# Kernel optimization log

Measured on AMD Instinct MI355X. Metric: run time of the kernel, lower is better.

The kernel has to match this reference:

```python
import jax, jax.numpy as jnp
import numpy as np

N_NODES = 50000
N_EDGES = 1600000
D = 128  # input_dim == hidden_dim


def glorot(key, shape):
    lim = float(np.sqrt(6.0 / (shape[0] + shape[1])))
    return jax.random.uniform(key, shape, jnp.float32, -lim, lim)


def setup_inputs() -> dict:
    key = jax.random.key(0)
    ks = jax.random.split(key, 10)
    x = jax.random.normal(ks[0], (N_NODES, D), jnp.float32)
    edge_index = jax.random.randint(ks[1], (2, N_EDGES), 0, N_NODES, jnp.int64)
    edge_attr = jax.random.normal(ks[2], (N_EDGES, D), jnp.float32)
    # SAGEConv params per layer: lin_l (W,b), lin_r (W, no bias)
    W1l = glorot(ks[3], (D, D)); b1l = jnp.zeros((D,), jnp.float32)
    W1r = glorot(ks[4], (D, D))
    W2l = glorot(ks[5], (D, D)); b2l = jnp.zeros((D,), jnp.float32)
    W2r = glorot(ks[6], (D, D))
    return {"x": x, "edge_index": edge_index, "edge_attr": edge_attr,
            "W1l": W1l, "b1l": b1l, "W1r": W1r,
            "W2l": W2l, "b2l": b2l, "W2r": W2r}


def sage_layer(z, src, dst, edge_attr, Wl, bl, Wr):
    # message: gather x_j, add edge_attr, relu  -> [E, D]
    msg = jax.nn.relu(z[src] + edge_attr)
    # mean aggregation at destination nodes
    agg = jax.ops.segment_sum(msg, dst, num_segments=N_NODES)
    cnt = jax.ops.segment_sum(jnp.ones((dst.shape[0], 1), z.dtype), dst,
                              num_segments=N_NODES)
    agg = agg / jnp.maximum(cnt, 1.0)
    # lin_l(agg) + lin_r(x) (root weight, no bias on lin_r)
    return agg @ Wl + bl + z @ Wr


def reference(x, edge_index, edge_attr, W1l, b1l, W1r, W2l, b2l, W2r):
    src, dst = edge_index[0], edge_index[1]
    z = sage_layer(x, src, dst, edge_attr, W1l, b1l, W1r)
    z = jax.nn.relu(z)  # activation between layers; dropout=0, normalize='none'
    z = sage_layer(z, src, dst, edge_attr, W2l, b2l, W2r)
    return z
```

## Files before the change

### kernel.cpp

```cpp
#include <hip/hip_runtime.h>

#define D 128

typedef __attribute__((ext_vector_type(8))) short bf16x8;
typedef __attribute__((ext_vector_type(4))) float f32x4;
typedef __attribute__((ext_vector_type(4))) unsigned short u16x4;
typedef __attribute__((ext_vector_type(4))) unsigned char u8x4;

__device__ inline unsigned short f2bf(float f) {
    union { float f; unsigned u; } v; v.f = f;
    unsigned r = v.u + 0x7FFF + ((v.u >> 16) & 1);
    return (unsigned short)(r >> 16);
}
__device__ inline float bf2f(unsigned short h) {
    union { unsigned u; float f; } v; v.u = ((unsigned)h) << 16; return v.f;
}
__device__ inline unsigned char f2fp8(float f) {
    unsigned u = __float_as_uint(f);
    unsigned s = (u >> 31) << 7;
    unsigned r = (u & 0x7fffffffu) + 0x7FFFF + ((u >> 20) & 1);
    int e = (int)(r >> 23) - 127;
    if (e < -6) return (unsigned char)s;
    return (unsigned char)(s | ((unsigned)(e + 7) << 3) | ((r >> 20) & 7));
}
__device__ inline float fp82f(unsigned c) {
    unsigned ef = (c >> 3) & 0xF, m = c & 7, s = c >> 7;
    unsigned nb = (s << 31) | ((ef + 120) << 23) | (m << 20);
    float nv = __uint_as_float(nb);
    float sv = (s ? -0.001953125f : 0.001953125f) * (float)m;
    return ef ? nv : sv;
}


__global__ __launch_bounds__(256) void prep_kernel(const float* __restrict__ x,
                                                   unsigned short* __restrict__ xb, int n4,
                                                   const int* __restrict__ dst,
                                                   int* __restrict__ cnt, int E,
                                                   const float* __restrict__ W1l,
                                                   const float* __restrict__ W1r,
                                                   const float* __restrict__ W2l,
                                                   const float* __restrict__ W2r,
                                                   unsigned short* __restrict__ Wt1,
                                                   unsigned short* __restrict__ Wt2,
                                                   int CAST_B, int CNT_B) {
    int b = blockIdx.x, tid = threadIdx.x;
    if (b < CAST_B) {
        int i = b * 256 + tid;
        if (i < n4) {
            float4 v = reinterpret_cast<const float4*>(x)[i];
            ushort4 r;
            r.x = f2bf(v.x); r.y = f2bf(v.y); r.z = f2bf(v.z); r.w = f2bf(v.w);
            reinterpret_cast<ushort4*>(xb)[i] = r;
        }
    } else if (b < CAST_B + CNT_B) {
        int e = (b - CAST_B) * 256 + tid;
        if (e < E) atomicAdd(&cnt[dst[e]], 1);
    } else {
        int c = b - CAST_B - CNT_B;
        int k = tid;
        float v1 = (k < 128) ? W1l[k * 128 + c] : W1r[(k - 128) * 128 + c];
        float v2 = (k < 128) ? W2l[k * 128 + c] : W2r[(k - 128) * 128 + c];
        Wt1[c * 256 + k] = f2bf(v1);
        Wt2[c * 256 + k] = f2bf(v2);
    }
}


__global__ __launch_bounds__(256) void psum_kernel(const int* __restrict__ cnt,
                                                   int* __restrict__ bsum, int n) {
    __shared__ int wsh[4];
    int b = blockIdx.x, tid = threadIdx.x;
    int i0 = b * 1024 + tid * 4;
    int s = 0;
    #pragma unroll
    for (int j = 0; j < 4; ++j) { int i = i0 + j; if (i < n) s += cnt[i]; }
    #pragma unroll
    for (int d = 1; d < 64; d <<= 1) s += __shfl_xor(s, d, 64);
    if ((tid & 63) == 0) wsh[tid >> 6] = s;
    __syncthreads();
    if (tid == 0) bsum[b] = wsh[0] + wsh[1] + wsh[2] + wsh[3];
}

__global__ __launch_bounds__(64) void bscan_kernel(const int* __restrict__ bsum,
                                                   int* __restrict__ bpre, int nb) {
    int t = threadIdx.x;
    int v = (t < nb) ? bsum[t] : 0;
    int sc = v;
    #pragma unroll
    for (int d = 1; d < 64; d <<= 1) { int u = __shfl_up(sc, d, 64); if (t >= d) sc += u; }
    if (t < nb) bpre[t] = sc - v;
}

__global__ __launch_bounds__(256) void fscan_kernel(const int* __restrict__ cnt,
                                                    const int* __restrict__ bpre,
                                                    int* __restrict__ off,
                                                    int* __restrict__ cursor, int n) {
    __shared__ int wsum[4];
    int b = blockIdx.x, tid = threadIdx.x;
    int lane = tid & 63, wv = tid >> 6;
    int i0 = b * 1024 + tid * 4;
    int v[4]; int s = 0;
    #pragma unroll
    for (int j = 0; j < 4; ++j) { int i = i0 + j; v[j] = (i < n) ? cnt[i] : 0; s += v[j]; }
    int sc = s;
    #pragma unroll
    for (int d = 1; d < 64; d <<= 1) { int u = __shfl_up(sc, d, 64); if (lane >= d) sc += u; }
    if (lane == 63) wsum[wv] = sc;
    __syncthreads();
    int wp = 0;
    for (int j = 0; j < wv; ++j) wp += wsum[j];
    int base = bpre[b] + wp + sc - s;
    #pragma unroll
    for (int j = 0; j < 4; ++j) {
        int i = i0 + j;
        if (i < n) { cursor[i] = base; off[i + 1] = base + v[j]; }
        base += v[j];
    }
    if (b == 0 && tid == 0) off[0] = 0;
}

__global__ __launch_bounds__(256) void fill_kernel(const int* __restrict__ src,
                                                   const int* __restrict__ dst,
                                                   int* __restrict__ cursor,
                                                   long long* __restrict__ pairs, int E) {
    int e = blockIdx.x * 256 + threadIdx.x;
    if (e < E) {
        int d = dst[e];
        int slot = atomicAdd(&cursor[d], 1);
        long long v = (long long)(unsigned)src[e] | ((long long)e << 32);
        __builtin_nontemporal_store(v, &pairs[slot]);
    }
}


template <int EA_FP8>
__global__ __launch_bounds__(256) void aggregate_kernel(const unsigned short* __restrict__ featb,
                                                        const float* __restrict__ ea,
                                                        unsigned char* __restrict__ eaq,
                                                        const int* __restrict__ off,
                                                        const long long* __restrict__ pairs,
                                                        unsigned short* __restrict__ aggb,
                                                        int N) {
    int nd = blockIdx.x * 4 + (threadIdx.x >> 6);
    if (nd >= N) return;
    int t = threadIdx.x & 63;
    int half = t >> 5, l32 = t & 31;
    int s = off[nd], e = off[nd + 1];
    float a0 = 0.f, a1 = 0.f, a2 = 0.f, a3 = 0.f;

    for (int b = s; b < e; b += 64) {
        int cnt = min(64, e - b);
        long long prl = (b + t < e) ? __builtin_nontemporal_load(&pairs[b + t]) : 0LL;
        int psrc = (int)prl;
        int peid = (int)(prl >> 32);

        auto fetch = [&](int idx, f32x4& ev, u16x4& xv) {
            int sidx = __shfl(psrc, idx, 64);
            int q = b + idx;
            if (EA_FP8) {
                u8x4 eq = __builtin_nontemporal_load(
                    reinterpret_cast<const u8x4*>(&eaq[(size_t)q * D + l32 * 4]));
                ev[0] = fp82f(eq[0]); ev[1] = fp82f(eq[1]);
                ev[2] = fp82f(eq[2]); ev[3] = fp82f(eq[3]);
            } else {
                int eidx = __shfl(peid, idx, 64);
                ev = __builtin_nontemporal_load(
                    reinterpret_cast<const f32x4*>(&ea[(size_t)eidx * D + l32 * 4]));
                u8x4 wq;
                wq[0] = f2fp8(ev[0]); wq[1] = f2fp8(ev[1]);
                wq[2] = f2fp8(ev[2]); wq[3] = f2fp8(ev[3]);
                __builtin_nontemporal_store(wq,
                    reinterpret_cast<u8x4*>(&eaq[(size_t)q * D + l32 * 4]));
            }
            xv = *reinterpret_cast<const u16x4*>(&featb[(size_t)sidx * D + l32 * 4]);
        };
        auto accum = [&](const f32x4& ev, const u16x4& xv) {
            a0 += fmaxf(bf2f(xv[0]) + ev[0], 0.f);
            a1 += fmaxf(bf2f(xv[1]) + ev[1], 0.f);
            a2 += fmaxf(bf2f(xv[2]) + ev[2], 0.f);
            a3 += fmaxf(bf2f(xv[3]) + ev[3], 0.f);
        };

        int p = 0;
        for (; p + 8 <= cnt; p += 8) {
            f32x4 e0, e1, e2, e3; u16x4 x0, x1, x2, x3;
            fetch(p + half, e0, x0);
            fetch(p + 2 + half, e1, x1);
            fetch(p + 4 + half, e2, x2);
            fetch(p + 6 + half, e3, x3);
            accum(e0, x0); accum(e1, x1); accum(e2, x2); accum(e3, x3);
        }
        if (p + 4 <= cnt) {
            f32x4 e0, e1; u16x4 x0, x1;
            fetch(p + half, e0, x0);
            fetch(p + 2 + half, e1, x1);
            accum(e0, x0); accum(e1, x1);
            p += 4;
        }
        if (p + 2 <= cnt) {
            f32x4 e0; u16x4 x0;
            fetch(p + half, e0, x0);
            accum(e0, x0);
            p += 2;
        }
        if (p < cnt) {
            f32x4 e0; u16x4 x0;
            fetch(p, e0, x0);
            if (half == 0) accum(e0, x0);
        }
    }

    a0 += __shfl_xor(a0, 32, 64);
    a1 += __shfl_xor(a1, 32, 64);
    a2 += __shfl_xor(a2, 32, 64);
    a3 += __shfl_xor(a3, 32, 64);
    int deg = e - s;
    float inv = 1.f / (float)(deg > 0 ? deg : 1);
    if (half == 0) {
        ushort4 r;
        r.x = f2bf(a0 * inv); r.y = f2bf(a1 * inv);
        r.z = f2bf(a2 * inv); r.w = f2bf(a3 * inv);
        *reinterpret_cast<ushort4*>(&aggb[(size_t)nd * D + l32 * 4]) = r;
    }
}


template <int RELU, int OUT_BF16>
__global__ __launch_bounds__(256) void gemm_mfma_kernel(const unsigned short* __restrict__ A1,
                                                        const unsigned short* __restrict__ A2,
                                                        const unsigned short* __restrict__ Wt,
                                                        const float* __restrict__ bias,
                                                        float* __restrict__ outf,
                                                        unsigned short* __restrict__ outb,
                                                        int MT, int N) {
    int tid = threadIdx.x;
    int w = tid >> 6;
    int l = tid & 63;
    int lr = l & 15;
    int lg = l >> 4;
    int c0 = w * 32;

    bf16x8 bfr[2][8];
    #pragma unroll
    for (int t = 0; t < 2; ++t)
        #pragma unroll
        for (int kc = 0; kc < 8; ++kc)
            bfr[t][kc] = *reinterpret_cast<const bf16x8*>(
                &Wt[(size_t)(c0 + t * 16 + lr) * 256 + kc * 32 + lg * 8]);

    for (int mt = blockIdx.x; mt < MT; mt += gridDim.x) {
        int r0 = mt * 32;
        f32x4 acc[2][2];
        #pragma unroll
        for (int tr = 0; tr < 2; ++tr)
            #pragma unroll
            for (int tc = 0; tc < 2; ++tc) acc[tr][tc] = {0.f, 0.f, 0.f, 0.f};

        #pragma unroll
        for (int kc = 0; kc < 8; ++kc) {
            const unsigned short* Ap = (kc < 4) ? A1 : A2;
            int k = (kc & 3) * 32 + lg * 8;
            bf16x8 af0 = *reinterpret_cast<const bf16x8*>(&Ap[(size_t)(r0 + lr) * D + k]);
            bf16x8 af1 = *reinterpret_cast<const bf16x8*>(&Ap[(size_t)(r0 + 16 + lr) * D + k]);
            acc[0][0] = __builtin_amdgcn_mfma_f32_16x16x32_bf16(af0, bfr[0][kc], acc[0][0], 0, 0, 0);
            acc[1][0] = __builtin_amdgcn_mfma_f32_16x16x32_bf16(af1, bfr[0][kc], acc[1][0], 0, 0, 0);
            acc[0][1] = __builtin_amdgcn_mfma_f32_16x16x32_bf16(af0, bfr[1][kc], acc[0][1], 0, 0, 0);
            acc[1][1] = __builtin_amdgcn_mfma_f32_16x16x32_bf16(af1, bfr[1][kc], acc[1][1], 0, 0, 0);
        }

        #pragma unroll
        for (int tc = 0; tc < 2; ++tc) {
            int col = c0 + tc * 16 + lr;
            float bv = bias[col];
            #pragma unroll
            for (int tr = 0; tr < 2; ++tr) {
                #pragma unroll
                for (int r = 0; r < 4; ++r) {
                    int row = r0 + tr * 16 + lg * 4 + r;
                    if (row < N) {
                        float v = acc[tr][tc][r] + bv;
                        if (RELU) v = fmaxf(v, 0.f);
                        if (OUT_BF16) outb[(size_t)row * D + col] = f2bf(v);
                        else outf[(size_t)row * D + col] = v;
                    }
                }
            }
        }
    }
}

extern "C" void kernel_launch(void* const* d_in, const int* in_sizes, int n_in,
                              void* d_out, int out_size, void* d_ws, size_t ws_size,
                              hipStream_t stream) {
    const float* x   = (const float*)d_in[0];
    const int*   ei  = (const int*)d_in[1];
    const float* ea  = (const float*)d_in[2];
    const float* W1l = (const float*)d_in[3];
    const float* b1l = (const float*)d_in[4];
    const float* W1r = (const float*)d_in[5];
    const float* W2l = (const float*)d_in[6];
    const float* b2l = (const float*)d_in[7];
    const float* W2r = (const float*)d_in[8];
    float* out = (float*)d_out;

    const int N = in_sizes[0] / D;
    const int E = in_sizes[1] / 2;
    const int NP = (N + 31) & ~31;
    const int* src = ei;
    const int* dst = ei + E;

    char* ws = (char*)d_ws;
    size_t o = 0;
    auto alloc = [&](size_t bytes) -> void* {
        void* p = ws + o;
        o = (o + bytes + 255) & ~(size_t)255;
        return p;
    };
    int*   cnt    = (int*)alloc((size_t)N * 4);
    int*   off    = (int*)alloc((size_t)(N + 1) * 4);
    int*   cursor = (int*)alloc((size_t)N * 4);
    int*   bsum   = (int*)alloc(256 * 4);
    int*   bpre   = (int*)alloc(256 * 4);
    long long* pairs = (long long*)alloc((size_t)E * 8);
    unsigned char* eaq = (unsigned char*)alloc((size_t)E * D);
    unsigned short* xb   = (unsigned short*)alloc((size_t)NP * D * 2);
    unsigned short* z1b  = (unsigned short*)alloc((size_t)NP * D * 2);
    unsigned short* aggb = (unsigned short*)alloc((size_t)NP * D * 2);
    unsigned short* Wt1  = (unsigned short*)alloc(128 * 256 * 2);
    unsigned short* Wt2  = (unsigned short*)alloc(128 * 256 * 2);
    (void)ws_size; (void)n_in; (void)out_size;

    const int MT = (N + 31) / 32;
    const int NB = (N + 1023) / 1024;
    const int AGB = (N + 3) / 4;
    const int n4 = N * D / 4;
    const int CAST_B = (n4 + 255) / 256;
    const int CNT_B = (E + 255) / 256;

    (void)hipMemsetAsync(cnt, 0, (size_t)N * 4, stream);
    prep_kernel<<<CAST_B + CNT_B + 128, 256, 0, stream>>>(x, xb, n4, dst, cnt, E,
                                                          W1l, W1r, W2l, W2r, Wt1, Wt2,
                                                          CAST_B, CNT_B);
    psum_kernel<<<NB, 256, 0, stream>>>(cnt, bsum, N);
    bscan_kernel<<<1, 64, 0, stream>>>(bsum, bpre, NB);
    fscan_kernel<<<NB, 256, 0, stream>>>(cnt, bpre, off, cursor, N);
    fill_kernel<<<(E + 255) / 256, 256, 0, stream>>>(src, dst, cursor, pairs, E);

    aggregate_kernel<0><<<AGB, 256, 0, stream>>>(xb, ea, eaq, off, pairs, aggb, N);
    gemm_mfma_kernel<1, 1><<<1024, 256, 0, stream>>>(aggb, xb, Wt1, b1l, nullptr, z1b, MT, N);

    aggregate_kernel<1><<<AGB, 256, 0, stream>>>(z1b, nullptr, eaq, off, pairs, aggb, N);
    gemm_mfma_kernel<0, 0><<<1024, 256, 0, stream>>>(aggb, z1b, Wt2, b2l, out, nullptr, MT, N);
}
```

Baseline: 607.1 us.

## Fuse neighbor aggregation with MFMA GEMM per layer and drop block-scan kernel

Each SAGE layer's mean aggregation and its dense linear transform now run in one kernel. A block aggregates 32 destination nodes into an XOR-swizzled LDS tile, then runs the bf16 MFMA GEMM from that tile plus the root features. This removes the intermediate aggregate buffer write and read and one launch per layer. The separate single-block prefix scan is folded into fscan, where each block sums the preceding block totals itself. Nontemporal hints on the pairs array are also dropped. In exchange, each wave handles 8 nodes serially and every block waits at a barrier for its slowest wave before the GEMM, so per-node degree imbalance can stall whole blocks.

```diff
diff --git a/kernel.cpp b/kernel.cpp
--- a/kernel.cpp
+++ b/kernel.cpp
@@ -81,23 +81,15 @@
     if (tid == 0) bsum[b] = wsh[0] + wsh[1] + wsh[2] + wsh[3];
 }
 
-__global__ __launch_bounds__(64) void bscan_kernel(const int* __restrict__ bsum,
-                                                   int* __restrict__ bpre, int nb) {
-    int t = threadIdx.x;
-    int v = (t < nb) ? bsum[t] : 0;
-    int sc = v;
-    #pragma unroll
-    for (int d = 1; d < 64; d <<= 1) { int u = __shfl_up(sc, d, 64); if (t >= d) sc += u; }
-    if (t < nb) bpre[t] = sc - v;
-}
-
 __global__ __launch_bounds__(256) void fscan_kernel(const int* __restrict__ cnt,
-                                                    const int* __restrict__ bpre,
+                                                    const int* __restrict__ bsum,
                                                     int* __restrict__ off,
                                                     int* __restrict__ cursor, int n) {
     __shared__ int wsum[4];
     int b = blockIdx.x, tid = threadIdx.x;
     int lane = tid & 63, wv = tid >> 6;
+    int bp = 0;
+    for (int j = 0; j < b; ++j) bp += bsum[j];
     int i0 = b * 1024 + tid * 4;
     int v[4]; int s = 0;
     #pragma unroll
@@ -109,7 +101,7 @@
     __syncthreads();
     int wp = 0;
     for (int j = 0; j < wv; ++j) wp += wsum[j];
-    int base = bpre[b] + wp + sc - s;
+    int base = bp + wp + sc - s;
     #pragma unroll
     for (int j = 0; j < 4; ++j) {
         int i = i0 + j;
@@ -127,162 +119,162 @@
     if (e < E) {
         int d = dst[e];
         int slot = atomicAdd(&cursor[d], 1);
-        long long v = (long long)(unsigned)src[e] | ((long long)e << 32);
-        __builtin_nontemporal_store(v, &pairs[slot]);
-    }
-}
-
-
-template <int EA_FP8>
-__global__ __launch_bounds__(256) void aggregate_kernel(const unsigned short* __restrict__ featb,
-                                                        const float* __restrict__ ea,
-                                                        unsigned char* __restrict__ eaq,
-                                                        const int* __restrict__ off,
-                                                        const long long* __restrict__ pairs,
-                                                        unsigned short* __restrict__ aggb,
-                                                        int N) {
-    int nd = blockIdx.x * 4 + (threadIdx.x >> 6);
-    if (nd >= N) return;
-    int t = threadIdx.x & 63;
-    int half = t >> 5, l32 = t & 31;
-    int s = off[nd], e = off[nd + 1];
-    float a0 = 0.f, a1 = 0.f, a2 = 0.f, a3 = 0.f;
-
-    for (int b = s; b < e; b += 64) {
-        int cnt = min(64, e - b);
-        long long prl = (b + t < e) ? __builtin_nontemporal_load(&pairs[b + t]) : 0LL;
-        int psrc = (int)prl;
-        int peid = (int)(prl >> 32);
-
-        auto fetch = [&](int idx, f32x4& ev, u16x4& xv) {
-            int sidx = __shfl(psrc, idx, 64);
-            int q = b + idx;
-            if (EA_FP8) {
-                u8x4 eq = __builtin_nontemporal_load(
-                    reinterpret_cast<const u8x4*>(&eaq[(size_t)q * D + l32 * 4]));
-                ev[0] = fp82f(eq[0]); ev[1] = fp82f(eq[1]);
-                ev[2] = fp82f(eq[2]); ev[3] = fp82f(eq[3]);
-            } else {
-                int eidx = __shfl(peid, idx, 64);
-                ev = __builtin_nontemporal_load(
-                    reinterpret_cast<const f32x4*>(&ea[(size_t)eidx * D + l32 * 4]));
-                u8x4 wq;
-                wq[0] = f2fp8(ev[0]); wq[1] = f2fp8(ev[1]);
-                wq[2] = f2fp8(ev[2]); wq[3] = f2fp8(ev[3]);
-                __builtin_nontemporal_store(wq,
-                    reinterpret_cast<u8x4*>(&eaq[(size_t)q * D + l32 * 4]));
+        pairs[slot] = (long long)(unsigned)src[e] | ((long long)e << 32);
+    }
+}
+
+
+template <int EA_FP8, int RELU, int OUT_BF16>
+__global__ __launch_bounds__(256) void fused_kernel(const unsigned short* __restrict__ featb,
+                                                    const float* __restrict__ ea,
+                                                    unsigned char* __restrict__ eaq,
+                                                    const int* __restrict__ off,
+                                                    const long long* __restrict__ pairs,
+                                                    const unsigned short* __restrict__ Wt,
+                                                    const float* __restrict__ bias,
+                                                    float* __restrict__ outf,
+                                                    unsigned short* __restrict__ outb,
+                                                    int N) {
+    __shared__ unsigned short sAgg[32][128];
+    int tid = threadIdx.x;
+    int w = tid >> 6, l = tid & 63;
+    int hf = l >> 5, l32 = l & 31;
+    int nbase = blockIdx.x * 32;
+
+    for (int i = 0; i < 8; ++i) {
+        int ndl = w * 8 + i;
+        int nd = nbase + ndl;
+        float a0 = 0.f, a1 = 0.f, a2 = 0.f, a3 = 0.f;
+        int deg = 0;
+        if (nd < N) {
+            int s = off[nd], e = off[nd + 1];
+            deg = e - s;
+            for (int b = s; b < e; b += 64) {
+                int cnt = min(64, e - b);
+                long long prl = (b + l < e) ? pairs[b + l] : 0LL;
+                int psrc = (int)prl;
+                int peid = (int)(prl >> 32);
+
+                auto fetch = [&](int idx, f32x4& ev, u16x4& xv) {
+                    int sidx = __shfl(psrc, idx, 64);
+                    int q = b + idx;
+                    if (EA_FP8) {
+                        u8x4 eq = __builtin_nontemporal_load(
+                            reinterpret_cast<const u8x4*>(&eaq[(size_t)q * D + l32 * 4]));
+                        ev[0] = fp82f(eq[0]); ev[1] = fp82f(eq[1]);
+                        ev[2] = fp82f(eq[2]); ev[3] = fp82f(eq[3]);
+                    } else {
+                        int eidx = __shfl(peid, idx, 64);
+                        ev = __builtin_nontemporal_load(
+                            reinterpret_cast<const f32x4*>(&ea[(size_t)eidx * D + l32 * 4]));
+                        u8x4 wq;
+                        wq[0] = f2fp8(ev[0]); wq[1] = f2fp8(ev[1]);
+                        wq[2] = f2fp8(ev[2]); wq[3] = f2fp8(ev[3]);
+                        __builtin_nontemporal_store(wq,
+                            reinterpret_cast<u8x4*>(&eaq[(size_t)q * D + l32 * 4]));
+                    }
+                    xv = *reinterpret_cast<const u16x4*>(&featb[(size_t)sidx * D + l32 * 4]);
+                };
+                auto accum = [&](const f32x4& ev, const u16x4& xv) {
+                    a0 += fmaxf(bf2f(xv[0]) + ev[0], 0.f);
+                    a1 += fmaxf(bf2f(xv[1]) + ev[1], 0.f);
+                    a2 += fmaxf(bf2f(xv[2]) + ev[2], 0.f);
+                    a3 += fmaxf(bf2f(xv[3]) + ev[3], 0.f);
+                };
+
+                int p = 0;
+                for (; p + 8 <= cnt; p += 8) {
+                    f32x4 e0, e1, e2, e3; u16x4 x0, x1, x2, x3;
+                    fetch(p + hf, e0, x0);
+                    fetch(p + 2 + hf, e1, x1);
+                    fetch(p + 4 + hf, e2, x2);
+                    fetch(p + 6 + hf, e3, x3);
+                    accum(e0, x0); accum(e1, x1); accum(e2, x2); accum(e3, x3);
+                }
+                if (p + 4 <= cnt) {
+                    f32x4 e0, e1; u16x4 x0, x1;
+                    fetch(p + hf, e0, x0);
+                    fetch(p + 2 + hf, e1, x1);
+                    accum(e0, x0); accum(e1, x1);
+                    p += 4;
+                }
+                if (p + 2 <= cnt) {
+                    f32x4 e0; u16x4 x0;
+                    fetch(p + hf, e0, x0);
+                    accum(e0, x0);
+                    p += 2;
+                }
+                if (p < cnt) {
+                    f32x4 e0; u16x4 x0;
+                    fetch(p, e0, x0);
+                    if (hf == 0) accum(e0, x0);
+                }
             }
-            xv = *reinterpret_cast<const u16x4*>(&featb[(size_t)sidx * D + l32 * 4]);
-        };
-        auto accum = [&](const f32x4& ev, const u16x4& xv) {
-            a0 += fmaxf(bf2f(xv[0]) + ev[0], 0.f);
-            a1 += fmaxf(bf2f(xv[1]) + ev[1], 0.f);
-            a2 += fmaxf(bf2f(xv[2]) + ev[2], 0.f);
-            a3 += fmaxf(bf2f(xv[3]) + ev[3], 0.f);
-        };
-
-        int p = 0;
-        for (; p + 8 <= cnt; p += 8) {
-            f32x4 e0, e1, e2, e3; u16x4 x0, x1, x2, x3;
-            fetch(p + half, e0, x0);
-            fetch(p + 2 + half, e1, x1);
-            fetch(p + 4 + half, e2, x2);
-            fetch(p + 6 + half, e3, x3);
-            accum(e0, x0); accum(e1, x1); accum(e2, x2); accum(e3, x3);
-        }
-        if (p + 4 <= cnt) {
-            f32x4 e0, e1; u16x4 x0, x1;
-            fetch(p + half, e0, x0);
-            fetch(p + 2 + half, e1, x1);
-            accum(e0, x0); accum(e1, x1);
-            p += 4;
-        }
-        if (p + 2 <= cnt) {
-            f32x4 e0; u16x4 x0;
-            fetch(p + half, e0, x0);
-            accum(e0, x0);
-            p += 2;
-        }
-        if (p < cnt) {
-            f32x4 e0; u16x4 x0;
-            fetch(p, e0, x0);
-            if (half == 0) accum(e0, x0);
-        }
-    }
-
-    a0 += __shfl_xor(a0, 32, 64);
-    a1 += __shfl_xor(a1, 32, 64);
-    a2 += __shfl_xor(a2, 32, 64);
-    a3 += __shfl_xor(a3, 32, 64);
-    int deg = e - s;
-    float inv = 1.f / (float)(deg > 0 ? deg : 1);
-    if (half == 0) {
-        ushort4 r;
-        r.x = f2bf(a0 * inv); r.y = f2bf(a1 * inv);
-        r.z = f2bf(a2 * inv); r.w = f2bf(a3 * inv);
-        *reinterpret_cast<ushort4*>(&aggb[(size_t)nd * D + l32 * 4]) = r;
-    }
-}
-
-
-template <int RELU, int OUT_BF16>
-__global__ __launch_bounds__(256) void gemm_mfma_kernel(const unsigned short* __restrict__ A1,
-                                                        const unsigned short* __restrict__ A2,
-                                                        const unsigned short* __restrict__ Wt,
-                                                        const float* __restrict__ bias,
-                                                        float* __restrict__ outf,
-                                                        unsigned short* __restrict__ outb,
-                                                        int MT, int N) {
-    int tid = threadIdx.x;
-    int w = tid >> 6;
-    int l = tid & 63;
-    int lr = l & 15;
-    int lg = l >> 4;
+        }
+        a0 += __shfl_xor(a0, 32, 64);
+        a1 += __shfl_xor(a1, 32, 64);
+        a2 += __shfl_xor(a2, 32, 64);
+        a3 += __shfl_xor(a3, 32, 64);
+        float inv = 1.f / (float)(deg > 0 ? deg : 1);
+        if (hf == 0) {
+            u16x4 r;
+            r[0] = f2bf(a0 * inv); r[1] = f2bf(a1 * inv);
+            r[2] = f2bf(a2 * inv); r[3] = f2bf(a3 * inv);
+            int colx = (l32 * 4) ^ ((ndl & 7) << 3);
+            *reinterpret_cast<u16x4*>(&sAgg[ndl][colx]) = r;
+        }
+    }
+    __syncthreads();
+
+    int lr = l & 15, lg = l >> 4;
     int c0 = w * 32;
 
     bf16x8 bfr[2][8];
     #pragma unroll
-    for (int t = 0; t < 2; ++t)
+    for (int t2 = 0; t2 < 2; ++t2)
         #pragma unroll
         for (int kc = 0; kc < 8; ++kc)
-            bfr[t][kc] = *reinterpret_cast<const bf16x8*>(
-                &Wt[(size_t)(c0 + t * 16 + lr) * 256 + kc * 32 + lg * 8]);
-
-    for (int mt = blockIdx.x; mt < MT; mt += gridDim.x) {
-        int r0 = mt * 32;
-        f32x4 acc[2][2];
+            bfr[t2][kc] = *reinterpret_cast<const bf16x8*>(
+                &Wt[(size_t)(c0 + t2 * 16 + lr) * 256 + kc * 32 + lg * 8]);
+
+    f32x4 acc[2][2];
+    #pragma unroll
+    for (int tr = 0; tr < 2; ++tr)
         #pragma unroll
-        for (int tr = 0; tr < 2; ++tr)
+        for (int tc = 0; tc < 2; ++tc) acc[tr][tc] = {0.f, 0.f, 0.f, 0.f};
+
+    #pragma unroll
+    for (int kc = 0; kc < 8; ++kc) {
+        int k = (kc & 3) * 32 + lg * 8;
+        bf16x8 af0, af1;
+        if (kc < 4) {
+            int r0x = lr, r1x = 16 + lr;
+            af0 = *reinterpret_cast<const bf16x8*>(&sAgg[r0x][k ^ ((r0x & 7) << 3)]);
+            af1 = *reinterpret_cast<const bf16x8*>(&sAgg[r1x][k ^ ((r1x & 7) << 3)]);
+        } else {
+            af0 = *reinterpret_cast<const bf16x8*>(&featb[(size_t)(nbase + lr) * D + k]);
+            af1 = *reinterpret_cast<const bf16x8*>(&featb[(size_t)(nbase + 16 + lr) * D + k]);
+        }
+        acc[0][0] = __builtin_amdgcn_mfma_f32_16x16x32_bf16(af0, bfr[0][kc], acc[0][0], 0, 0, 0);
+        acc[1][0] = __builtin_amdgcn_mfma_f32_16x16x32_bf16(af1, bfr[0][kc], acc[1][0], 0, 0, 0);
+        acc[0][1] = __builtin_amdgcn_mfma_f32_16x16x32_bf16(af0, bfr[1][kc], acc[0][1], 0, 0, 0);
+        acc[1][1] = __builtin_amdgcn_mfma_f32_16x16x32_bf16(af1, bfr[1][kc], acc[1][1], 0, 0, 0);
+    }
+
+    #pragma unroll
+    for (int tc = 0; tc < 2; ++tc) {
+        int col = c0 + tc * 16 + lr;
+        float bv = bias[col];
+        #pragma unroll
+        for (int tr = 0; tr < 2; ++tr) {
             #pragma unroll
-            for (int tc = 0; tc < 2; ++tc) acc[tr][tc] = {0.f, 0.f, 0.f, 0.f};
-
-        #pragma unroll
-        for (int kc = 0; kc < 8; ++kc) {
-            const unsigned short* Ap = (kc < 4) ? A1 : A2;
-            int k = (kc & 3) * 32 + lg * 8;
-            bf16x8 af0 = *reinterpret_cast<const bf16x8*>(&Ap[(size_t)(r0 + lr) * D + k]);
-            bf16x8 af1 = *reinterpret_cast<const bf16x8*>(&Ap[(size_t)(r0 + 16 + lr) * D + k]);
-            acc[0][0] = __builtin_amdgcn_mfma_f32_16x16x32_bf16(af0, bfr[0][kc], acc[0][0], 0, 0, 0);
-            acc[1][0] = __builtin_amdgcn_mfma_f32_16x16x32_bf16(af1, bfr[0][kc], acc[1][0], 0, 0, 0);
-            acc[0][1] = __builtin_amdgcn_mfma_f32_16x16x32_bf16(af0, bfr[1][kc], acc[0][1], 0, 0, 0);
-            acc[1][1] = __builtin_amdgcn_mfma_f32_16x16x32_bf16(af1, bfr[1][kc], acc[1][1], 0, 0, 0);
-        }
-
-        #pragma unroll
-        for (int tc = 0; tc < 2; ++tc) {
-            int col = c0 + tc * 16 + lr;
-            float bv = bias[col];
-            #pragma unroll
-            for (int tr = 0; tr < 2; ++tr) {
-                #pragma unroll
-                for (int r = 0; r < 4; ++r) {
-                    int row = r0 + tr * 16 + lg * 4 + r;
-                    if (row < N) {
-                        float v = acc[tr][tc][r] + bv;
-                        if (RELU) v = fmaxf(v, 0.f);
-                        if (OUT_BF16) outb[(size_t)row * D + col] = f2bf(v);
-                        else outf[(size_t)row * D + col] = v;
-                    }
+            for (int r = 0; r < 4; ++r) {
+                int row = nbase + tr * 16 + lg * 4 + r;
+                if (row < N) {
+                    float v = acc[tr][tc][r] + bv;
+                    if (RELU) v = fmaxf(v, 0.f);
+                    if (OUT_BF16) outb[(size_t)row * D + col] = f2bf(v);
+                    else outf[(size_t)row * D + col] = v;
                 }
             }
         }
@@ -320,19 +312,16 @@
     int*   off    = (int*)alloc((size_t)(N + 1) * 4);
     int*   cursor = (int*)alloc((size_t)N * 4);
     int*   bsum   = (int*)alloc(256 * 4);
-    int*   bpre   = (int*)alloc(256 * 4);
     long long* pairs = (long long*)alloc((size_t)E * 8);
     unsigned char* eaq = (unsigned char*)alloc((size_t)E * D);
     unsigned short* xb   = (unsigned short*)alloc((size_t)NP * D * 2);
     unsigned short* z1b  = (unsigned short*)alloc((size_t)NP * D * 2);
-    unsigned short* aggb = (unsigned short*)alloc((size_t)NP * D * 2);
     unsigned short* Wt1  = (unsigned short*)alloc(128 * 256 * 2);
     unsigned short* Wt2  = (unsigned short*)alloc(128 * 256 * 2);
     (void)ws_size; (void)n_in; (void)out_size;
 
-    const int MT = (N + 31) / 32;
     const int NB = (N + 1023) / 1024;
-    const int AGB = (N + 3) / 4;
+    const int FB = (N + 31) / 32;
     const int n4 = N * D / 4;
     const int CAST_B = (n4 + 255) / 256;
     const int CNT_B = (E + 255) / 256;
@@ -342,13 +331,11 @@
                                                           W1l, W1r, W2l, W2r, Wt1, Wt2,
                                                           CAST_B, CNT_B);
     psum_kernel<<<NB, 256, 0, stream>>>(cnt, bsum, N);
-    bscan_kernel<<<1, 64, 0, stream>>>(bsum, bpre, NB);
-    fscan_kernel<<<NB, 256, 0, stream>>>(cnt, bpre, off, cursor, N);
+    fscan_kernel<<<NB, 256, 0, stream>>>(cnt, bsum, off, cursor, N);
     fill_kernel<<<(E + 255) / 256, 256, 0, stream>>>(src, dst, cursor, pairs, E);
 
-    aggregate_kernel<0><<<AGB, 256, 0, stream>>>(xb, ea, eaq, off, pairs, aggb, N);
-    gemm_mfma_kernel<1, 1><<<1024, 256, 0, stream>>>(aggb, xb, Wt1, b1l, nullptr, z1b, MT, N);
-
-    aggregate_kernel<1><<<AGB, 256, 0, stream>>>(z1b, nullptr, eaq, off, pairs, aggb, N);
-    gemm_mfma_kernel<0, 0><<<1024, 256, 0, stream>>>(aggb, z1b, Wt2, b2l, out, nullptr, MT, N);
-}
+    fused_kernel<0, 1, 1><<<FB, 256, 0, stream>>>(xb, ea, eaq, off, pairs,
+                                                  Wt1, b1l, nullptr, z1b, N);
+    fused_kernel<1, 0, 0><<<FB, 256, 0, stream>>>(z1b, nullptr, eaq, off, pairs,
+                                                  Wt2, b2l, out, nullptr, N);
+}
```

New measurement: 630.6 us. 1.04x slower.

## Quantize and permute edge attributes during CSR fill instead of first aggregation

Applied to the files above, without the earlier changes.

The fill kernel now reads edge_attr coalesced in edge order, converts it to fp8 and writes it directly into CSR-sorted slots, alongside a 4-byte source index. This replaces the random-order fp32 edge_attr gather via stored edge ids inside the first aggregation pass. The separate block-scan kernel is dropped, and each fscan block sums prior block totals serially. Both aggregation passes now share a single fp8-only code path, at the cost of scattered writes and one atomic per edge done per half-wave in the fill stage.

```diff
diff --git a/kernel.cpp b/kernel.cpp
--- a/kernel.cpp
+++ b/kernel.cpp
@@ -81,23 +81,15 @@
     if (tid == 0) bsum[b] = wsh[0] + wsh[1] + wsh[2] + wsh[3];
 }
 
-__global__ __launch_bounds__(64) void bscan_kernel(const int* __restrict__ bsum,
-                                                   int* __restrict__ bpre, int nb) {
-    int t = threadIdx.x;
-    int v = (t < nb) ? bsum[t] : 0;
-    int sc = v;
-    #pragma unroll
-    for (int d = 1; d < 64; d <<= 1) { int u = __shfl_up(sc, d, 64); if (t >= d) sc += u; }
-    if (t < nb) bpre[t] = sc - v;
-}
-
 __global__ __launch_bounds__(256) void fscan_kernel(const int* __restrict__ cnt,
-                                                    const int* __restrict__ bpre,
+                                                    const int* __restrict__ bsum,
                                                     int* __restrict__ off,
                                                     int* __restrict__ cursor, int n) {
     __shared__ int wsum[4];
     int b = blockIdx.x, tid = threadIdx.x;
     int lane = tid & 63, wv = tid >> 6;
+    int bp = 0;
+    for (int j = 0; j < b; ++j) bp += bsum[j];
     int i0 = b * 1024 + tid * 4;
     int v[4]; int s = 0;
     #pragma unroll
@@ -109,7 +101,7 @@
     __syncthreads();
     int wp = 0;
     for (int j = 0; j < wv; ++j) wp += wsum[j];
-    int base = bpre[b] + wp + sc - s;
+    int base = bp + wp + sc - s;
     #pragma unroll
     for (int j = 0; j < 4; ++j) {
         int i = i0 + j;
@@ -119,26 +111,37 @@
     if (b == 0 && tid == 0) off[0] = 0;
 }
 
+
 __global__ __launch_bounds__(256) void fill_kernel(const int* __restrict__ src,
                                                    const int* __restrict__ dst,
                                                    int* __restrict__ cursor,
-                                                   long long* __restrict__ pairs, int E) {
-    int e = blockIdx.x * 256 + threadIdx.x;
-    if (e < E) {
-        int d = dst[e];
-        int slot = atomicAdd(&cursor[d], 1);
-        long long v = (long long)(unsigned)src[e] | ((long long)e << 32);
-        __builtin_nontemporal_store(v, &pairs[slot]);
-    }
-}
-
-
-template <int EA_FP8>
+                                                   int* __restrict__ pairsrc,
+                                                   const float* __restrict__ ea,
+                                                   unsigned char* __restrict__ eaq, int E) {
+    int gw = (blockIdx.x * 256 + threadIdx.x) >> 6;
+    int nw = (gridDim.x * 256) >> 6;
+    int t = threadIdx.x & 63;
+    int hf = t >> 5, l32 = t & 31;
+    for (int e0 = gw * 2; e0 < E; e0 += nw * 2) {
+        int e = e0 + hf;
+        int slot = 0;
+        if (l32 == 0) slot = atomicAdd(&cursor[dst[e]], 1);
+        slot = __shfl(slot, hf << 5, 64);
+        f32x4 ev = __builtin_nontemporal_load(
+            reinterpret_cast<const f32x4*>(&ea[(size_t)e * D + l32 * 4]));
+        u8x4 q;
+        q[0] = f2fp8(ev[0]); q[1] = f2fp8(ev[1]);
+        q[2] = f2fp8(ev[2]); q[3] = f2fp8(ev[3]);
+        *reinterpret_cast<u8x4*>(&eaq[(size_t)slot * D + l32 * 4]) = q;
+        if (l32 == 0) pairsrc[slot] = src[e];
+    }
+}
+
+
 __global__ __launch_bounds__(256) void aggregate_kernel(const unsigned short* __restrict__ featb,
-                                                        const float* __restrict__ ea,
-                                                        unsigned char* __restrict__ eaq,
+                                                        const unsigned char* __restrict__ eaq,
                                                         const int* __restrict__ off,
-                                                        const long long* __restrict__ pairs,
+                                                        const int* __restrict__ pairsrc,
                                                         unsigned short* __restrict__ aggb,
                                                         int N) {
     int nd = blockIdx.x * 4 + (threadIdx.x >> 6);
@@ -150,28 +153,15 @@
 
     for (int b = s; b < e; b += 64) {
         int cnt = min(64, e - b);
-        long long prl = (b + t < e) ? __builtin_nontemporal_load(&pairs[b + t]) : 0LL;
-        int psrc = (int)prl;
-        int peid = (int)(prl >> 32);
+        int psrc = (b + t < e) ? __builtin_nontemporal_load(&pairsrc[b + t]) : 0;
 
         auto fetch = [&](int idx, f32x4& ev, u16x4& xv) {
             int sidx = __shfl(psrc, idx, 64);
             int q = b + idx;
-            if (EA_FP8) {
-                u8x4 eq = __builtin_nontemporal_load(
-                    reinterpret_cast<const u8x4*>(&eaq[(size_t)q * D + l32 * 4]));
-                ev[0] = fp82f(eq[0]); ev[1] = fp82f(eq[1]);
-                ev[2] = fp82f(eq[2]); ev[3] = fp82f(eq[3]);
-            } else {
-                int eidx = __shfl(peid, idx, 64);
-                ev = __builtin_nontemporal_load(
-                    reinterpret_cast<const f32x4*>(&ea[(size_t)eidx * D + l32 * 4]));
-                u8x4 wq;
-                wq[0] = f2fp8(ev[0]); wq[1] = f2fp8(ev[1]);
-                wq[2] = f2fp8(ev[2]); wq[3] = f2fp8(ev[3]);
-                __builtin_nontemporal_store(wq,
-                    reinterpret_cast<u8x4*>(&eaq[(size_t)q * D + l32 * 4]));
-            }
+            u8x4 eq = __builtin_nontemporal_load(
+                reinterpret_cast<const u8x4*>(&eaq[(size_t)q * D + l32 * 4]));
+            ev[0] = fp82f(eq[0]); ev[1] = fp82f(eq[1]);
+            ev[2] = fp82f(eq[2]); ev[3] = fp82f(eq[3]);
             xv = *reinterpret_cast<const u16x4*>(&featb[(size_t)sidx * D + l32 * 4]);
         };
         auto accum = [&](const f32x4& ev, const u16x4& xv) {
@@ -217,10 +207,10 @@
     int deg = e - s;
     float inv = 1.f / (float)(deg > 0 ? deg : 1);
     if (half == 0) {
-        ushort4 r;
-        r.x = f2bf(a0 * inv); r.y = f2bf(a1 * inv);
-        r.z = f2bf(a2 * inv); r.w = f2bf(a3 * inv);
-        *reinterpret_cast<ushort4*>(&aggb[(size_t)nd * D + l32 * 4]) = r;
+        u16x4 r;
+        r[0] = f2bf(a0 * inv); r[1] = f2bf(a1 * inv);
+        r[2] = f2bf(a2 * inv); r[3] = f2bf(a3 * inv);
+        *reinterpret_cast<u16x4*>(&aggb[(size_t)nd * D + l32 * 4]) = r;
     }
 }
 
@@ -316,12 +306,11 @@
         o = (o + bytes + 255) & ~(size_t)255;
         return p;
     };
-    int*   cnt    = (int*)alloc((size_t)N * 4);
-    int*   off    = (int*)alloc((size_t)(N + 1) * 4);
-    int*   cursor = (int*)alloc((size_t)N * 4);
-    int*   bsum   = (int*)alloc(256 * 4);
-    int*   bpre   = (int*)alloc(256 * 4);
-    long long* pairs = (long long*)alloc((size_t)E * 8);
+    int*   cnt     = (int*)alloc((size_t)N * 4);
+    int*   off     = (int*)alloc((size_t)(N + 1) * 4);
+    int*   cursor  = (int*)alloc((size_t)N * 4);
+    int*   bsum    = (int*)alloc(256 * 4);
+    int*   pairsrc = (int*)alloc((size_t)E * 4);
     unsigned char* eaq = (unsigned char*)alloc((size_t)E * D);
     unsigned short* xb   = (unsigned short*)alloc((size_t)NP * D * 2);
     unsigned short* z1b  = (unsigned short*)alloc((size_t)NP * D * 2);
@@ -342,13 +331,12 @@
                                                           W1l, W1r, W2l, W2r, Wt1, Wt2,
                                                           CAST_B, CNT_B);
     psum_kernel<<<NB, 256, 0, stream>>>(cnt, bsum, N);
-    bscan_kernel<<<1, 64, 0, stream>>>(bsum, bpre, NB);
-    fscan_kernel<<<NB, 256, 0, stream>>>(cnt, bpre, off, cursor, N);
-    fill_kernel<<<(E + 255) / 256, 256, 0, stream>>>(src, dst, cursor, pairs, E);
-
-    aggregate_kernel<0><<<AGB, 256, 0, stream>>>(xb, ea, eaq, off, pairs, aggb, N);
+    fscan_kernel<<<NB, 256, 0, stream>>>(cnt, bsum, off, cursor, N);
+    fill_kernel<<<4096, 256, 0, stream>>>(src, dst, cursor, pairsrc, ea, eaq, E);
+
+    aggregate_kernel<<<AGB, 256, 0, stream>>>(xb, eaq, off, pairsrc, aggb, N);
     gemm_mfma_kernel<1, 1><<<1024, 256, 0, stream>>>(aggb, xb, Wt1, b1l, nullptr, z1b, MT, N);
 
-    aggregate_kernel<1><<<AGB, 256, 0, stream>>>(z1b, nullptr, eaq, off, pairs, aggb, N);
+    aggregate_kernel<<<AGB, 256, 0, stream>>>(z1b, eaq, off, pairsrc, aggb, N);
     gemm_mfma_kernel<0, 0><<<1024, 256, 0, stream>>>(aggb, z1b, Wt2, b2l, out, nullptr, MT, N);
 }
```

New measurement: 621.6 us. 1.02x slower.
